# Performance work log

Measured on AMD Instinct MI355X. Metric: run time of the kernel, lower is better.

Reference implementation:

```python
import jax, jax.numpy as jnp
import numpy as np
import math

NH, NKV, D = 32, 8, 128  # query heads, kv heads, head_dim
ROPE_THETA = 10000.0


def _rotate_half(x):
    x1, x2 = jnp.split(x, 2, axis=-1)
    return jnp.concatenate([-x2, x1], axis=-1)


def _rope_cache(position_ids):
    # position_ids: [B, S] int -> cos, sin: [B, S, D]
    inv_freq = 1.0 / (ROPE_THETA ** (jnp.arange(0, D, 2, dtype=jnp.float32) / D))
    freqs = position_ids.astype(jnp.float32)[..., None] * inv_freq  # [B,S,D/2]
    emb = jnp.concatenate([freqs, freqs], axis=-1)  # [B,S,D]
    return jnp.cos(emb), jnp.sin(emb)


def setup_inputs() -> dict:
    key = jax.random.key(0)
    k0, k1, k2, k3, k4 = jax.random.split(key, 5)
    B, S, H = 1, 2048, 4096
    scale = 0.02
    return {
        "hidden_states": jax.random.normal(k0, (B, S, H), jnp.float32),
        "position_ids": jnp.broadcast_to(jnp.arange(S, dtype=jnp.int32), (B, S)),
        "Wq": jax.random.normal(k1, (H, NH * D), jnp.float32) * scale,
        "Wk": jax.random.normal(k2, (H, NKV * D), jnp.float32) * scale,
        "Wv": jax.random.normal(k3, (H, NKV * D), jnp.float32) * scale,
        "Wo": jax.random.normal(k4, (NH * D, H), jnp.float32) * scale,
    }


def reference(hidden_states, position_ids, Wq, Wk, Wv, Wo):
    B, S, H = hidden_states.shape
    # QKV projections, move heads front: [B, H, S, D]
    Q = (hidden_states @ Wq).reshape(B, S, NH, D).transpose(0, 2, 1, 3)
    K = (hidden_states @ Wk).reshape(B, S, NKV, D).transpose(0, 2, 1, 3)
    V = (hidden_states @ Wv).reshape(B, S, NKV, D).transpose(0, 2, 1, 3)
    # RoPE
    cos, sin = _rope_cache(position_ids)  # [B,S,D]
    cos, sin = cos[:, None], sin[:, None]  # broadcast over heads
    Q = Q * cos + _rotate_half(Q) * sin
    K = K * cos + _rotate_half(K) * sin
    # GQA: repeat kv heads to match query heads
    g = NH // NKV
    K = jnp.repeat(K, g, axis=1)
    V = jnp.repeat(V, g, axis=1)
    # scaled QK^T with causal mask (mask=True -> keep, else finfo.min)
    scores = jnp.einsum("bhqd,bhkd->bhqk", Q, K) / math.sqrt(D)
    causal = jnp.tril(jnp.ones((S, S), dtype=bool))
    scores = jnp.where(causal, scores, jnp.finfo(scores.dtype).min)
    probs = jax.nn.softmax(scores.astype(jnp.float32), axis=-1).astype(Q.dtype)
    attn = jnp.einsum("bhqk,bhkd->bhqd", probs, V)
    attn = attn.transpose(0, 2, 1, 3).reshape(B, S, NH * D)
    return attn @ Wo
```

## Files before the change

kernel.cpp:

```cpp
#include <hip/hip_runtime.h>
#include <hip/hip_bf16.h>
#include <math.h>

typedef __bf16 bf16;
typedef __bf16 bf16x8 __attribute__((ext_vector_type(8)));
typedef float f32x4 __attribute__((ext_vector_type(4)));

#define GLB __attribute__((address_space(1)))
#define LDSAS __attribute__((address_space(3)))

__global__ void probe_dtype(const unsigned int* __restrict__ X, int* __restrict__ flag) {
  int t = threadIdx.x;
  int cnt = 0;
  for (int i = t; i < 512; i += 64) {
    unsigned int e = (X[i] >> 7) & 0xFF;
    cnt += (e >= 110 && e <= 135) ? 1 : 0;
  }
#pragma unroll
  for (int off = 32; off > 0; off >>= 1) cnt += __shfl_down(cnt, off, 64);
  if (t == 0) flag[0] = (cnt < 256) ? 1 : 0;
}

__global__ void cast_to_bf16(const void* __restrict__ X, bf16* __restrict__ Y,
                             const int* __restrict__ flag, int n) {
  const int i = (blockIdx.x * 256 + threadIdx.x) * 4;
  if (i >= n) return;
  if (flag[0]) {
    const float* xf = (const float*)X;
#pragma unroll
    for (int j = 0; j < 4; ++j) Y[i + j] = (bf16)xf[i + j];
  } else {
    const bf16* xb = (const bf16*)X;
#pragma unroll
    for (int j = 0; j < 4; ++j) Y[i + j] = xb[i + j];
  }
}

__global__ void transpose_to_bf16(const void* __restrict__ W, bf16* __restrict__ Wt,
                                  const int* __restrict__ flag, int K, int N) {
  __shared__ bf16 tile[32][34];
  const int n0 = blockIdx.x * 32, k0 = blockIdx.y * 32;
  const int tx = threadIdx.x, ty = threadIdx.y;
  const int f = flag[0];
#pragma unroll
  for (int j = 0; j < 4; ++j) {
    const size_t idx = (size_t)(k0 + ty + j * 8) * N + n0 + tx;
    tile[ty + j * 8][tx] = f ? (bf16)((const float*)W)[idx] : ((const bf16*)W)[idx];
  }
  __syncthreads();
#pragma unroll
  for (int j = 0; j < 4; ++j)
    Wt[(size_t)(n0 + ty + j * 8) * K + k0 + tx] = tile[tx][ty + j * 8];
}

__global__ void transpose_v(const bf16* __restrict__ V, bf16* __restrict__ Vt) {
  __shared__ bf16 tile[32][34];
  const int v0 = blockIdx.x * 32, s0 = blockIdx.y * 32;
  const int tx = threadIdx.x, ty = threadIdx.y;
#pragma unroll
  for (int j = 0; j < 4; ++j)
    tile[ty + j * 8][tx] = V[(size_t)(s0 + ty + j * 8) * 6144 + v0 + tx];
  __syncthreads();
#pragma unroll
  for (int j = 0; j < 4; ++j)
    Vt[(size_t)(v0 + ty + j * 8) * 2048 + s0 + tx] = tile[tx][ty + j * 8];
}

__global__ __launch_bounds__(256, 2) void gemm_bt(
    const bf16* __restrict__ A, const bf16* __restrict__ Bt,
    void* __restrict__ C, const int* __restrict__ flagp, int M, int N, int K) {
  __shared__ bf16 As[128 * 32];
  __shared__ bf16 Bs[128 * 32];
  const int t = threadIdx.x;
  const int m0 = blockIdx.y * 128, n0 = blockIdx.x * 128;
  const int lane = t & 63, n16 = lane & 15, quad = lane >> 4;
  const int w = t >> 6, wrow = w >> 1, wcol = w & 1;

  f32x4 acc[4][4] = {};
  const int colA = (t & 3) * 8;
  const int rA = t >> 2;

  for (int k0 = 0; k0 < K; k0 += 32) {
#pragma unroll
    for (int i = 0; i < 2; ++i) {
      const int elem = i * 2048 + t * 8;
      const int row = i * 64 + rA;
      __builtin_amdgcn_global_load_lds(
          (const GLB void*)(A + (size_t)(m0 + row) * K + k0 + colA),
          (LDSAS void*)(&As[elem]), 16, 0, 0);
      __builtin_amdgcn_global_load_lds(
          (const GLB void*)(Bt + (size_t)(n0 + row) * K + k0 + colA),
          (LDSAS void*)(&Bs[elem]), 16, 0, 0);
    }
    __syncthreads();
    bf16x8 af[4], bfr[4];
#pragma unroll
    for (int i = 0; i < 4; ++i) {
      af[i] = *(const bf16x8*)&As[(wrow * 64 + i * 16 + n16) * 32 + quad * 8];
      bfr[i] = *(const bf16x8*)&Bs[(wcol * 64 + i * 16 + n16) * 32 + quad * 8];
    }
#pragma unroll
    for (int mi = 0; mi < 4; ++mi)
#pragma unroll
      for (int ni = 0; ni < 4; ++ni)
        acc[mi][ni] = __builtin_amdgcn_mfma_f32_16x16x32_bf16(
            af[mi], bfr[ni], acc[mi][ni], 0, 0, 0);
    __syncthreads();
  }
  const bool f32out = (flagp != nullptr) && (flagp[0] != 0);
  if (f32out) {
    float* Cf = (float*)C;
#pragma unroll
    for (int mi = 0; mi < 4; ++mi)
#pragma unroll
      for (int ni = 0; ni < 4; ++ni) {
        const int r0 = m0 + wrow * 64 + mi * 16 + quad * 4;
        const int c = n0 + wcol * 64 + ni * 16 + n16;
#pragma unroll
        for (int r = 0; r < 4; ++r) Cf[(size_t)(r0 + r) * N + c] = acc[mi][ni][r];
      }
  } else {
    bf16* Cb = (bf16*)C;
#pragma unroll
    for (int mi = 0; mi < 4; ++mi)
#pragma unroll
      for (int ni = 0; ni < 4; ++ni) {
        const int r0 = m0 + wrow * 64 + mi * 16 + quad * 4;
        const int c = n0 + wcol * 64 + ni * 16 + n16;
#pragma unroll
        for (int r = 0; r < 4; ++r) Cb[(size_t)(r0 + r) * N + c] = (bf16)acc[mi][ni][r];
      }
  }
}

__global__ void rope_kernel(bf16* __restrict__ X, const int* __restrict__ pos,
                            int heads, int stride, int col0) {
  const int idx = blockIdx.x * 256 + threadIdx.x;
  const int i = idx & 63;
  const int hh = (idx >> 6) % heads;
  const int s = idx / (64 * heads);
  bf16* px = X + (size_t)s * stride + col0 + hh * 128 + i;
  const float x1 = (float)px[0], x2 = (float)px[64];
  const float p = (float)pos[s];
  const float inv = exp2f((float)i * -0.2076205088f);
  float sn, cs;
  sincosf(p * inv, &sn, &cs);
  px[0] = (bf16)(x1 * cs - x2 * sn);
  px[64] = (bf16)(x2 * cs + x1 * sn);
}

__global__ __launch_bounds__(256) void flash_attn(
    const bf16* __restrict__ QKV, const bf16* __restrict__ Vt_g,
    bf16* __restrict__ O) {
  __shared__ bf16 Ks[64 * 136];
  __shared__ bf16 Vs[128 * 64];
  __shared__ bf16 Ps[64 * 72];
  const int pairp = blockIdx.x;
  const int h = blockIdx.y, hkv = h >> 2;
  const int t = threadIdx.x, w = t >> 6, lane = t & 63;
  const int n16 = lane & 15, quad = lane >> 4;
  const bf16* Qp = QKV + h * 128;
  const bf16* Kp = QKV + 4096 + hkv * 128;
  const int srow = t >> 4, scol = (t & 15) * 8;
  const int vc = t & 7;

  for (int pass = 0; pass < 2; ++pass) {
    const int qt = (pass == 0) ? pairp : 31 - pairp;
    bf16x8 qa[4];
    {
      const bf16* qrow = Qp + (size_t)(qt * 64 + w * 16 + n16) * 6144 + quad * 8;
#pragma unroll
      for (int kf = 0; kf < 4; ++kf) qa[kf] = *(const bf16x8*)(qrow + kf * 32);
    }
    f32x4 o[8] = {};
    float m_[4] = {-1e30f, -1e30f, -1e30f, -1e30f};
    float l_[4] = {0.f, 0.f, 0.f, 0.f};

    for (int kt = 0; kt <= qt; ++kt) {
#pragma unroll
      for (int j = 0; j < 4; ++j) {
        const int rr = j * 16 + srow;
        *(bf16x8*)&Ks[rr * 136 + scol] =
            *(const bf16x8*)(Kp + (size_t)(kt * 64 + rr) * 6144 + scol);
      }
#pragma unroll
      for (int it = 0; it < 4; ++it) {
        const int d = it * 32 + (t >> 3);
        const bf16x8 vv = *(const bf16x8*)(
            Vt_g + (size_t)(hkv * 128 + d) * 2048 + kt * 64 + vc * 8);
        *(bf16x8*)&Vs[d * 64 + ((vc ^ (d & 7)) * 8)] = vv;
      }
      __syncthreads();

      float p[4][4];
      const bool diag = (kt == qt);
#pragma unroll
      for (int ns = 0; ns < 4; ++ns) {
        f32x4 c = {};
#pragma unroll
        for (int kf = 0; kf < 4; ++kf)
          c = __builtin_amdgcn_mfma_f32_16x16x32_bf16(
              qa[kf],
              *(const bf16x8*)&Ks[(ns * 16 + n16) * 136 + kf * 32 + quad * 8],
              c, 0, 0, 0);
        if (diag) {
          const int kvi = ns * 16 + n16;
          const int ql = w * 16 + quad * 4;
#pragma unroll
          for (int r = 0; r < 4; ++r)
            p[ns][r] = (kvi > ql + r) ? -1e30f : c[r] * 0.08838834764831845f;
        } else {
#pragma unroll
          for (int r = 0; r < 4; ++r) p[ns][r] = c[r] * 0.08838834764831845f;
        }
      }
      float alpha[4];
#pragma unroll
      for (int r = 0; r < 4; ++r) {
        float rmax = fmaxf(fmaxf(p[0][r], p[1][r]), fmaxf(p[2][r], p[3][r]));
#pragma unroll
        for (int off = 1; off < 16; off <<= 1)
          rmax = fmaxf(rmax, __shfl_xor(rmax, off, 64));
        const float mn = fmaxf(m_[r], rmax);
        alpha[r] = __expf(m_[r] - mn);
        float rs = 0.f;
#pragma unroll
        for (int ns = 0; ns < 4; ++ns) {
          const float e = __expf(p[ns][r] - mn);
          p[ns][r] = e;
          rs += e;
        }
#pragma unroll
        for (int off = 1; off < 16; off <<= 1) rs += __shfl_xor(rs, off, 64);
        l_[r] = l_[r] * alpha[r] + rs;
        m_[r] = mn;
      }
#pragma unroll
      for (int dt = 0; dt < 8; ++dt)
#pragma unroll
        for (int r = 0; r < 4; ++r) o[dt][r] *= alpha[r];
#pragma unroll
      for (int ns = 0; ns < 4; ++ns)
#pragma unroll
        for (int r = 0; r < 4; ++r)
          Ps[(w * 16 + quad * 4 + r) * 72 + ns * 16 + n16] = (bf16)p[ns][r];
      __syncthreads();
      const bf16x8 a0 = *(const bf16x8*)&Ps[(w * 16 + n16) * 72 + quad * 8];
      const bf16x8 a1 = *(const bf16x8*)&Ps[(w * 16 + n16) * 72 + 32 + quad * 8];
#pragma unroll
      for (int dt = 0; dt < 8; ++dt) {
        const int d = dt * 16 + n16;
        const int s7 = d & 7;
        const bf16x8 b0 = *(const bf16x8*)&Vs[d * 64 + ((quad ^ s7) * 8)];
        o[dt] = __builtin_amdgcn_mfma_f32_16x16x32_bf16(a0, b0, o[dt], 0, 0, 0);
        const bf16x8 b1 = *(const bf16x8*)&Vs[d * 64 + (((4 + quad) ^ s7) * 8)];
        o[dt] = __builtin_amdgcn_mfma_f32_16x16x32_bf16(a1, b1, o[dt], 0, 0, 0);
      }
      __syncthreads();
    }
    float linv[4];
#pragma unroll
    for (int r = 0; r < 4; ++r) linv[r] = 1.f / l_[r];
#pragma unroll
    for (int dt = 0; dt < 8; ++dt)
#pragma unroll
      for (int r = 0; r < 4; ++r) {
        const int qi = qt * 64 + w * 16 + quad * 4 + r;
        O[(size_t)qi * 4096 + h * 128 + dt * 16 + n16] = (bf16)(o[dt][r] * linv[r]);
      }
  }
}

extern "C" void kernel_launch(void* const* d_in, const int* in_sizes, int n_in,
                              void* d_out, int out_size, void* d_ws, size_t ws_size,
                              hipStream_t stream) {
  (void)in_sizes; (void)n_in; (void)out_size; (void)ws_size;
  const void* X = d_in[0];
  const int* pos = (const int*)d_in[1];
  const void* Wq = d_in[2];
  const void* Wk = d_in[3];
  const void* Wv = d_in[4];
  const void* Wo = d_in[5];

  char* ws = (char*)d_ws;
  const size_t MB = 1ull << 20;
  int* flag   = (int*)(ws + 0);
  bf16* Xb    = (bf16*)(ws + 1 * MB);
  bf16* attn  = (bf16*)(ws + 1 * MB);
  bf16* Wqkvt = (bf16*)(ws + 17 * MB);
  bf16* Wot   = (bf16*)(ws + 65 * MB);
  bf16* QKV   = (bf16*)(ws + 97 * MB);
  bf16* Vt_g  = (bf16*)(ws + 121 * MB);

  probe_dtype<<<1, 64, 0, stream>>>((const unsigned int*)X, flag);
  cast_to_bf16<<<8192, 256, 0, stream>>>(X, Xb, flag, 2048 * 4096);

  const dim3 tb(32, 8);
  transpose_to_bf16<<<dim3(128, 128), tb, 0, stream>>>(Wq, Wqkvt, flag, 4096, 4096);
  transpose_to_bf16<<<dim3(32, 128), tb, 0, stream>>>(Wk, Wqkvt + (size_t)4096 * 4096, flag, 4096, 1024);
  transpose_to_bf16<<<dim3(32, 128), tb, 0, stream>>>(Wv, Wqkvt + (size_t)5120 * 4096, flag, 4096, 1024);
  transpose_to_bf16<<<dim3(128, 128), tb, 0, stream>>>(Wo, Wot, flag, 4096, 4096);

  gemm_bt<<<dim3(48, 16), 256, 0, stream>>>(Xb, Wqkvt, QKV, nullptr, 2048, 6144, 4096);

  rope_kernel<<<16384, 256, 0, stream>>>(QKV, pos, 32, 6144, 0);
  rope_kernel<<<4096, 256, 0, stream>>>(QKV, pos, 8, 6144, 4096);

  transpose_v<<<dim3(32, 64), tb, 0, stream>>>(QKV + 5120, Vt_g);

  flash_attn<<<dim3(16, 32), 256, 0, stream>>>(QKV, Vt_g, attn);

  gemm_bt<<<dim3(32, 16), 256, 0, stream>>>(attn, Wot, d_out, flag, 2048, 4096, 4096);
}
```

Measured before the change: 563.3 us.

## Fuse prep kernels, swizzle GEMM LDS, merge RoPE, widen flash-attn query tiles

Merges the input cast and four weight transposes into one prep kernel, and folds the two RoPE launches into one covering the 40 Q+K heads. The GEMM LDS layout gets an XOR swizzle to cut bank conflicts. Flash attention moves from paired 64-row passes to 128-row query tiles per block with a 1D grid ordered longest-first, so each K/V tile load is shared by more queries and one barrier per tile is removed. The price is more registers for the doubled accumulators and per-group causal skipping inside the key loop.

```diff
diff --git a/kernel.cpp b/kernel.cpp
--- a/kernel.cpp
+++ b/kernel.cpp
@@ -21,27 +21,37 @@
   if (t == 0) flag[0] = (cnt < 256) ? 1 : 0;
 }
 
-__global__ void cast_to_bf16(const void* __restrict__ X, bf16* __restrict__ Y,
-                             const int* __restrict__ flag, int n) {
-  const int i = (blockIdx.x * 256 + threadIdx.x) * 4;
-  if (i >= n) return;
-  if (flag[0]) {
-    const float* xf = (const float*)X;
-#pragma unroll
-    for (int j = 0; j < 4; ++j) Y[i + j] = (bf16)xf[i + j];
+__global__ void prep_weights(const void* __restrict__ Wq, const void* __restrict__ Wk,
+                             const void* __restrict__ Wv, const void* __restrict__ Wo,
+                             const void* __restrict__ X,
+                             bf16* __restrict__ Wqkvt, bf16* __restrict__ Wot,
+                             bf16* __restrict__ Xb, const int* __restrict__ flag) {
+  const int f = flag[0];
+  const int tx = threadIdx.x, ty = threadIdx.y;
+  __shared__ bf16 tile[32][34];
+  int b = blockIdx.x;
+  const void* W;
+  bf16* out;
+  int N, bx, by;
+  if (b < 16384) {
+    W = Wq; out = Wqkvt; N = 4096; bx = b & 127; by = b >> 7;
+  } else if (b < 20480) {
+    b -= 16384; W = Wk; out = Wqkvt + (size_t)4096 * 4096; N = 1024; bx = b & 31; by = b >> 5;
+  } else if (b < 24576) {
+    b -= 20480; W = Wv; out = Wqkvt + (size_t)5120 * 4096; N = 1024; bx = b & 31; by = b >> 5;
+  } else if (b < 40960) {
+    b -= 24576; W = Wo; out = Wot; N = 4096; bx = b & 127; by = b >> 7;
   } else {
-    const bf16* xb = (const bf16*)X;
-#pragma unroll
-    for (int j = 0; j < 4; ++j) Y[i + j] = xb[i + j];
-  }
-}
-
-__global__ void transpose_to_bf16(const void* __restrict__ W, bf16* __restrict__ Wt,
-                                  const int* __restrict__ flag, int K, int N) {
-  __shared__ bf16 tile[32][34];
-  const int n0 = blockIdx.x * 32, k0 = blockIdx.y * 32;
-  const int tx = threadIdx.x, ty = threadIdx.y;
-  const int f = flag[0];
+    b -= 40960;
+    const int x0 = (b & 127) * 32, s0 = (b >> 7) * 32;
+#pragma unroll
+    for (int j = 0; j < 4; ++j) {
+      const size_t idx = (size_t)(s0 + ty + j * 8) * 4096 + x0 + tx;
+      Xb[idx] = f ? (bf16)((const float*)X)[idx] : ((const bf16*)X)[idx];
+    }
+    return;
+  }
+  const int n0 = bx * 32, k0 = by * 32;
 #pragma unroll
   for (int j = 0; j < 4; ++j) {
     const size_t idx = (size_t)(k0 + ty + j * 8) * N + n0 + tx;
@@ -50,7 +60,7 @@
   __syncthreads();
 #pragma unroll
   for (int j = 0; j < 4; ++j)
-    Wt[(size_t)(n0 + ty + j * 8) * K + k0 + tx] = tile[tx][ty + j * 8];
+    out[(size_t)(n0 + ty + j * 8) * 4096 + k0 + tx] = tile[tx][ty + j * 8];
 }
 
 __global__ void transpose_v(const bf16* __restrict__ V, bf16* __restrict__ Vt) {
@@ -77,8 +87,10 @@
   const int w = t >> 6, wrow = w >> 1, wcol = w & 1;
 
   f32x4 acc[4][4] = {};
-  const int colA = (t & 3) * 8;
+  const int colA = (((t & 3) ^ ((t >> 3) & 3))) * 8;
   const int rA = t >> 2;
+  const int sw = (n16 >> 1) & 3;
+  const int rdoff = ((quad ^ sw) * 8);
 
   for (int k0 = 0; k0 < K; k0 += 32) {
 #pragma unroll
@@ -96,8 +108,8 @@
     bf16x8 af[4], bfr[4];
 #pragma unroll
     for (int i = 0; i < 4; ++i) {
-      af[i] = *(const bf16x8*)&As[(wrow * 64 + i * 16 + n16) * 32 + quad * 8];
-      bfr[i] = *(const bf16x8*)&Bs[(wcol * 64 + i * 16 + n16) * 32 + quad * 8];
+      af[i] = *(const bf16x8*)&As[(wrow * 64 + i * 16 + n16) * 32 + rdoff];
+      bfr[i] = *(const bf16x8*)&Bs[(wcol * 64 + i * 16 + n16) * 32 + rdoff];
     }
 #pragma unroll
     for (int mi = 0; mi < 4; ++mi)
@@ -134,12 +146,12 @@
 }
 
 __global__ void rope_kernel(bf16* __restrict__ X, const int* __restrict__ pos,
-                            int heads, int stride, int col0) {
+                            int heads, int stride) {
   const int idx = blockIdx.x * 256 + threadIdx.x;
   const int i = idx & 63;
   const int hh = (idx >> 6) % heads;
   const int s = idx / (64 * heads);
-  bf16* px = X + (size_t)s * stride + col0 + hh * 128 + i;
+  bf16* px = X + (size_t)s * stride + hh * 128 + i;
   const float x1 = (float)px[0], x2 = (float)px[64];
   const float p = (float)pos[s];
   const float inv = exp2f((float)i * -0.2076205088f);
@@ -154,9 +166,10 @@
     bf16* __restrict__ O) {
   __shared__ bf16 Ks[64 * 136];
   __shared__ bf16 Vs[128 * 64];
-  __shared__ bf16 Ps[64 * 72];
-  const int pairp = blockIdx.x;
-  const int h = blockIdx.y, hkv = h >> 2;
+  __shared__ bf16 Ps[128 * 72];
+  const int x = blockIdx.x;
+  const int h = x & 31, hkv = h >> 2;
+  const int qt = (x < 256) ? (15 - (x >> 5)) : ((x - 256) >> 5);
   const int t = threadIdx.x, w = t >> 6, lane = t & 63;
   const int n16 = lane & 15, quad = lane >> 4;
   const bf16* Qp = QKV + h * 128;
@@ -164,48 +177,55 @@
   const int srow = t >> 4, scol = (t & 15) * 8;
   const int vc = t & 7;
 
-  for (int pass = 0; pass < 2; ++pass) {
-    const int qt = (pass == 0) ? pairp : 31 - pairp;
-    bf16x8 qa[4];
-    {
-      const bf16* qrow = Qp + (size_t)(qt * 64 + w * 16 + n16) * 6144 + quad * 8;
-#pragma unroll
-      for (int kf = 0; kf < 4; ++kf) qa[kf] = *(const bf16x8*)(qrow + kf * 32);
-    }
-    f32x4 o[8] = {};
-    float m_[4] = {-1e30f, -1e30f, -1e30f, -1e30f};
-    float l_[4] = {0.f, 0.f, 0.f, 0.f};
-
-    for (int kt = 0; kt <= qt; ++kt) {
-#pragma unroll
-      for (int j = 0; j < 4; ++j) {
-        const int rr = j * 16 + srow;
-        *(bf16x8*)&Ks[rr * 136 + scol] =
-            *(const bf16x8*)(Kp + (size_t)(kt * 64 + rr) * 6144 + scol);
-      }
-#pragma unroll
-      for (int it = 0; it < 4; ++it) {
-        const int d = it * 32 + (t >> 3);
-        const bf16x8 vv = *(const bf16x8*)(
-            Vt_g + (size_t)(hkv * 128 + d) * 2048 + kt * 64 + vc * 8);
-        *(bf16x8*)&Vs[d * 64 + ((vc ^ (d & 7)) * 8)] = vv;
-      }
-      __syncthreads();
-
+  bf16x8 qa[2][4];
+#pragma unroll
+  for (int g = 0; g < 2; ++g) {
+    const bf16* qrow = Qp + (size_t)(qt * 128 + w * 32 + g * 16 + n16) * 6144 + quad * 8;
+#pragma unroll
+    for (int kf = 0; kf < 4; ++kf) qa[g][kf] = *(const bf16x8*)(qrow + kf * 32);
+  }
+  f32x4 o[2][8] = {};
+  float m_[2][4], l_[2][4];
+#pragma unroll
+  for (int g = 0; g < 2; ++g)
+#pragma unroll
+    for (int r = 0; r < 4; ++r) { m_[g][r] = -1e30f; l_[g][r] = 0.f; }
+
+  const int nkt = 2 * qt + 2;
+  for (int kt = 0; kt < nkt; ++kt) {
+#pragma unroll
+    for (int j = 0; j < 4; ++j) {
+      const int rr = j * 16 + srow;
+      *(bf16x8*)&Ks[rr * 136 + scol] =
+          *(const bf16x8*)(Kp + (size_t)(kt * 64 + rr) * 6144 + scol);
+    }
+#pragma unroll
+    for (int it = 0; it < 4; ++it) {
+      const int d = it * 32 + (t >> 3);
+      const bf16x8 vv = *(const bf16x8*)(
+          Vt_g + (size_t)(hkv * 128 + d) * 2048 + kt * 64 + vc * 8);
+      *(bf16x8*)&Vs[d * 64 + ((vc ^ (d & 7)) * 8)] = vv;
+    }
+    __syncthreads();
+
+#pragma unroll
+    for (int g = 0; g < 2; ++g) {
+      const int bq = qt * 128 + w * 32 + g * 16;
+      if (kt * 64 > bq + 15) continue;
       float p[4][4];
-      const bool diag = (kt == qt);
+      const bool needMask = (kt * 64 + 63 > bq);
 #pragma unroll
       for (int ns = 0; ns < 4; ++ns) {
         f32x4 c = {};
 #pragma unroll
         for (int kf = 0; kf < 4; ++kf)
           c = __builtin_amdgcn_mfma_f32_16x16x32_bf16(
-              qa[kf],
+              qa[g][kf],
               *(const bf16x8*)&Ks[(ns * 16 + n16) * 136 + kf * 32 + quad * 8],
               c, 0, 0, 0);
-        if (diag) {
-          const int kvi = ns * 16 + n16;
-          const int ql = w * 16 + quad * 4;
+        if (needMask) {
+          const int kvi = kt * 64 + ns * 16 + n16;
+          const int ql = bq + quad * 4;
 #pragma unroll
           for (int r = 0; r < 4; ++r)
             p[ns][r] = (kvi > ql + r) ? -1e30f : c[r] * 0.08838834764831845f;
@@ -221,8 +241,8 @@
 #pragma unroll
         for (int off = 1; off < 16; off <<= 1)
           rmax = fmaxf(rmax, __shfl_xor(rmax, off, 64));
-        const float mn = fmaxf(m_[r], rmax);
-        alpha[r] = __expf(m_[r] - mn);
+        const float mn = fmaxf(m_[g][r], rmax);
+        alpha[r] = __expf(m_[g][r] - mn);
         float rs = 0.f;
 #pragma unroll
         for (int ns = 0; ns < 4; ++ns) {
@@ -232,41 +252,43 @@
         }
 #pragma unroll
         for (int off = 1; off < 16; off <<= 1) rs += __shfl_xor(rs, off, 64);
-        l_[r] = l_[r] * alpha[r] + rs;
-        m_[r] = mn;
+        l_[g][r] = l_[g][r] * alpha[r] + rs;
+        m_[g][r] = mn;
       }
 #pragma unroll
       for (int dt = 0; dt < 8; ++dt)
 #pragma unroll
-        for (int r = 0; r < 4; ++r) o[dt][r] *= alpha[r];
+        for (int r = 0; r < 4; ++r) o[g][dt][r] *= alpha[r];
 #pragma unroll
       for (int ns = 0; ns < 4; ++ns)
 #pragma unroll
         for (int r = 0; r < 4; ++r)
-          Ps[(w * 16 + quad * 4 + r) * 72 + ns * 16 + n16] = (bf16)p[ns][r];
-      __syncthreads();
-      const bf16x8 a0 = *(const bf16x8*)&Ps[(w * 16 + n16) * 72 + quad * 8];
-      const bf16x8 a1 = *(const bf16x8*)&Ps[(w * 16 + n16) * 72 + 32 + quad * 8];
+          Ps[(w * 32 + g * 16 + quad * 4 + r) * 72 + ns * 16 + n16] = (bf16)p[ns][r];
+      const bf16x8 a0 = *(const bf16x8*)&Ps[(w * 32 + g * 16 + n16) * 72 + quad * 8];
+      const bf16x8 a1 = *(const bf16x8*)&Ps[(w * 32 + g * 16 + n16) * 72 + 32 + quad * 8];
 #pragma unroll
       for (int dt = 0; dt < 8; ++dt) {
         const int d = dt * 16 + n16;
         const int s7 = d & 7;
         const bf16x8 b0 = *(const bf16x8*)&Vs[d * 64 + ((quad ^ s7) * 8)];
-        o[dt] = __builtin_amdgcn_mfma_f32_16x16x32_bf16(a0, b0, o[dt], 0, 0, 0);
+        o[g][dt] = __builtin_amdgcn_mfma_f32_16x16x32_bf16(a0, b0, o[g][dt], 0, 0, 0);
         const bf16x8 b1 = *(const bf16x8*)&Vs[d * 64 + (((4 + quad) ^ s7) * 8)];
-        o[dt] = __builtin_amdgcn_mfma_f32_16x16x32_bf16(a1, b1, o[dt], 0, 0, 0);
-      }
-      __syncthreads();
-    }
+        o[g][dt] = __builtin_amdgcn_mfma_f32_16x16x32_bf16(a1, b1, o[g][dt], 0, 0, 0);
+      }
+    }
+    __syncthreads();
+  }
+#pragma unroll
+  for (int g = 0; g < 2; ++g) {
     float linv[4];
 #pragma unroll
-    for (int r = 0; r < 4; ++r) linv[r] = 1.f / l_[r];
+    for (int r = 0; r < 4; ++r) linv[r] = 1.f / l_[g][r];
 #pragma unroll
     for (int dt = 0; dt < 8; ++dt)
 #pragma unroll
       for (int r = 0; r < 4; ++r) {
-        const int qi = qt * 64 + w * 16 + quad * 4 + r;
-        O[(size_t)qi * 4096 + h * 128 + dt * 16 + n16] = (bf16)(o[dt][r] * linv[r]);
+        const int qi = qt * 128 + w * 32 + g * 16 + quad * 4 + r;
+        O[(size_t)qi * 4096 + h * 128 + dt * 16 + n16] = (bf16)(o[g][dt][r] * linv[r]);
       }
   }
 }
@@ -293,22 +315,17 @@
   bf16* Vt_g  = (bf16*)(ws + 121 * MB);
 
   probe_dtype<<<1, 64, 0, stream>>>((const unsigned int*)X, flag);
-  cast_to_bf16<<<8192, 256, 0, stream>>>(X, Xb, flag, 2048 * 4096);
-
-  const dim3 tb(32, 8);
-  transpose_to_bf16<<<dim3(128, 128), tb, 0, stream>>>(Wq, Wqkvt, flag, 4096, 4096);
-  transpose_to_bf16<<<dim3(32, 128), tb, 0, stream>>>(Wk, Wqkvt + (size_t)4096 * 4096, flag, 4096, 1024);
-  transpose_to_bf16<<<dim3(32, 128), tb, 0, stream>>>(Wv, Wqkvt + (size_t)5120 * 4096, flag, 4096, 1024);
-  transpose_to_bf16<<<dim3(128, 128), tb, 0, stream>>>(Wo, Wot, flag, 4096, 4096);
+
+  prep_weights<<<49152, dim3(32, 8), 0, stream>>>(Wq, Wk, Wv, Wo, X,
+                                                  Wqkvt, Wot, Xb, flag);
 
   gemm_bt<<<dim3(48, 16), 256, 0, stream>>>(Xb, Wqkvt, QKV, nullptr, 2048, 6144, 4096);
 
-  rope_kernel<<<16384, 256, 0, stream>>>(QKV, pos, 32, 6144, 0);
-  rope_kernel<<<4096, 256, 0, stream>>>(QKV, pos, 8, 6144, 4096);
-
-  transpose_v<<<dim3(32, 64), tb, 0, stream>>>(QKV + 5120, Vt_g);
-
-  flash_attn<<<dim3(16, 32), 256, 0, stream>>>(QKV, Vt_g, attn);
+  rope_kernel<<<20480, 256, 0, stream>>>(QKV, pos, 40, 6144);
+
+  transpose_v<<<dim3(32, 64), dim3(32, 8), 0, stream>>>(QKV + 5120, Vt_g);
+
+  flash_attn<<<512, 256, 0, stream>>>(QKV, Vt_g, attn);
 
   gemm_bt<<<dim3(32, 16), 256, 0, stream>>>(attn, Wot, d_out, flag, 2048, 4096, 4096);
 }
```

New measurement: 615.3 us. 9.2% more time.

## Double-buffer flash-attn K/V via LDS DMA, swizzle GEMM LDS, merge prep kernels

Applied to the files above, without the earlier changes.

Flash attention now stages K and V tiles with direct global-to-LDS loads into double buffers, so the next tile loads while the current one is computed. It uses XOR-swizzled layouts and drops two barriers per iteration. The GEMM gets an XOR swizzle on its LDS tiles to reduce bank conflicts. The cast and weight-transpose kernels are merged into one launch, and the two RoPE launches become one. This relies on the compiler waiting for the asynchronous LDS loads before each barrier, and on Ps staying wave-private, which is a correctness risk if either assumption fails.

```diff
diff --git a/kernel.cpp b/kernel.cpp
--- a/kernel.cpp
+++ b/kernel.cpp
@@ -21,27 +21,37 @@
   if (t == 0) flag[0] = (cnt < 256) ? 1 : 0;
 }
 
-__global__ void cast_to_bf16(const void* __restrict__ X, bf16* __restrict__ Y,
-                             const int* __restrict__ flag, int n) {
-  const int i = (blockIdx.x * 256 + threadIdx.x) * 4;
-  if (i >= n) return;
-  if (flag[0]) {
-    const float* xf = (const float*)X;
-#pragma unroll
-    for (int j = 0; j < 4; ++j) Y[i + j] = (bf16)xf[i + j];
+__global__ void prep_weights(const void* __restrict__ Wq, const void* __restrict__ Wk,
+                             const void* __restrict__ Wv, const void* __restrict__ Wo,
+                             const void* __restrict__ X,
+                             bf16* __restrict__ Wqkvt, bf16* __restrict__ Wot,
+                             bf16* __restrict__ Xb, const int* __restrict__ flag) {
+  const int f = flag[0];
+  const int tx = threadIdx.x, ty = threadIdx.y;
+  __shared__ bf16 tile[32][34];
+  int b = blockIdx.x;
+  const void* W;
+  bf16* out;
+  int N, bx, by;
+  if (b < 16384) {
+    W = Wq; out = Wqkvt; N = 4096; bx = b & 127; by = b >> 7;
+  } else if (b < 20480) {
+    b -= 16384; W = Wk; out = Wqkvt + (size_t)4096 * 4096; N = 1024; bx = b & 31; by = b >> 5;
+  } else if (b < 24576) {
+    b -= 20480; W = Wv; out = Wqkvt + (size_t)5120 * 4096; N = 1024; bx = b & 31; by = b >> 5;
+  } else if (b < 40960) {
+    b -= 24576; W = Wo; out = Wot; N = 4096; bx = b & 127; by = b >> 7;
   } else {
-    const bf16* xb = (const bf16*)X;
-#pragma unroll
-    for (int j = 0; j < 4; ++j) Y[i + j] = xb[i + j];
-  }
-}
-
-__global__ void transpose_to_bf16(const void* __restrict__ W, bf16* __restrict__ Wt,
-                                  const int* __restrict__ flag, int K, int N) {
-  __shared__ bf16 tile[32][34];
-  const int n0 = blockIdx.x * 32, k0 = blockIdx.y * 32;
-  const int tx = threadIdx.x, ty = threadIdx.y;
-  const int f = flag[0];
+    b -= 40960;
+    const int x0 = (b & 127) * 32, s0 = (b >> 7) * 32;
+#pragma unroll
+    for (int j = 0; j < 4; ++j) {
+      const size_t idx = (size_t)(s0 + ty + j * 8) * 4096 + x0 + tx;
+      Xb[idx] = f ? (bf16)((const float*)X)[idx] : ((const bf16*)X)[idx];
+    }
+    return;
+  }
+  const int n0 = bx * 32, k0 = by * 32;
 #pragma unroll
   for (int j = 0; j < 4; ++j) {
     const size_t idx = (size_t)(k0 + ty + j * 8) * N + n0 + tx;
@@ -50,7 +60,7 @@
   __syncthreads();
 #pragma unroll
   for (int j = 0; j < 4; ++j)
-    Wt[(size_t)(n0 + ty + j * 8) * K + k0 + tx] = tile[tx][ty + j * 8];
+    out[(size_t)(n0 + ty + j * 8) * 4096 + k0 + tx] = tile[tx][ty + j * 8];
 }
 
 __global__ void transpose_v(const bf16* __restrict__ V, bf16* __restrict__ Vt) {
@@ -77,8 +87,10 @@
   const int w = t >> 6, wrow = w >> 1, wcol = w & 1;
 
   f32x4 acc[4][4] = {};
-  const int colA = (t & 3) * 8;
+  const int colA = (((t & 3) ^ ((t >> 3) & 3))) * 8;
   const int rA = t >> 2;
+  const int sw = (n16 >> 1) & 3;
+  const int rdoff = ((quad ^ sw) * 8);
 
   for (int k0 = 0; k0 < K; k0 += 32) {
 #pragma unroll
@@ -96,8 +108,8 @@
     bf16x8 af[4], bfr[4];
 #pragma unroll
     for (int i = 0; i < 4; ++i) {
-      af[i] = *(const bf16x8*)&As[(wrow * 64 + i * 16 + n16) * 32 + quad * 8];
-      bfr[i] = *(const bf16x8*)&Bs[(wcol * 64 + i * 16 + n16) * 32 + quad * 8];
+      af[i] = *(const bf16x8*)&As[(wrow * 64 + i * 16 + n16) * 32 + rdoff];
+      bfr[i] = *(const bf16x8*)&Bs[(wcol * 64 + i * 16 + n16) * 32 + rdoff];
     }
 #pragma unroll
     for (int mi = 0; mi < 4; ++mi)
@@ -134,12 +146,12 @@
 }
 
 __global__ void rope_kernel(bf16* __restrict__ X, const int* __restrict__ pos,
-                            int heads, int stride, int col0) {
+                            int heads, int stride) {
   const int idx = blockIdx.x * 256 + threadIdx.x;
   const int i = idx & 63;
   const int hh = (idx >> 6) % heads;
   const int s = idx / (64 * heads);
-  bf16* px = X + (size_t)s * stride + col0 + hh * 128 + i;
+  bf16* px = X + (size_t)s * stride + hh * 128 + i;
   const float x1 = (float)px[0], x2 = (float)px[64];
   const float p = (float)pos[s];
   const float inv = exp2f((float)i * -0.2076205088f);
@@ -152,8 +164,8 @@
 __global__ __launch_bounds__(256) void flash_attn(
     const bf16* __restrict__ QKV, const bf16* __restrict__ Vt_g,
     bf16* __restrict__ O) {
-  __shared__ bf16 Ks[64 * 136];
-  __shared__ bf16 Vs[128 * 64];
+  __shared__ bf16 Ks[2][64 * 128];
+  __shared__ bf16 Vs[2][128 * 64];
   __shared__ bf16 Ps[64 * 72];
   const int pairp = blockIdx.x;
   const int h = blockIdx.y, hkv = h >> 2;
@@ -161,8 +173,10 @@
   const int n16 = lane & 15, quad = lane >> 4;
   const bf16* Qp = QKV + h * 128;
   const bf16* Kp = QKV + 4096 + hkv * 128;
-  const int srow = t >> 4, scol = (t & 15) * 8;
-  const int vc = t & 7;
+  const bf16* Vp = Vt_g + (size_t)hkv * 128 * 2048;
+
+  const int krow = t >> 4, kg = t & 15;
+  const int vd = t >> 3, vg = t & 7;
 
   for (int pass = 0; pass < 2; ++pass) {
     const int qt = (pass == 0) ? pairp : 31 - pairp;
@@ -176,24 +190,36 @@
     float m_[4] = {-1e30f, -1e30f, -1e30f, -1e30f};
     float l_[4] = {0.f, 0.f, 0.f, 0.f};
 
+    __syncthreads();
+
+    auto stage = [&](int kt, int buf) {
+#pragma unroll
+      for (int j = 0; j < 4; ++j) {
+        const int row = j * 16 + krow;
+        const int g = kg ^ (row & 7);
+        __builtin_amdgcn_global_load_lds(
+            (const GLB void*)(Kp + (size_t)(kt * 64 + row) * 6144 + g * 8),
+            (LDSAS void*)(&Ks[buf][j * 2048 + t * 8]), 16, 0, 0);
+      }
+#pragma unroll
+      for (int j = 0; j < 4; ++j) {
+        const int d = j * 32 + vd;
+        const int g = vg ^ (d & 7);
+        __builtin_amdgcn_global_load_lds(
+            (const GLB void*)(Vp + (size_t)d * 2048 + kt * 64 + g * 8),
+            (LDSAS void*)(&Vs[buf][j * 2048 + t * 8]), 16, 0, 0);
+      }
+    };
+
+    stage(0, 0);
     for (int kt = 0; kt <= qt; ++kt) {
-#pragma unroll
-      for (int j = 0; j < 4; ++j) {
-        const int rr = j * 16 + srow;
-        *(bf16x8*)&Ks[rr * 136 + scol] =
-            *(const bf16x8*)(Kp + (size_t)(kt * 64 + rr) * 6144 + scol);
-      }
-#pragma unroll
-      for (int it = 0; it < 4; ++it) {
-        const int d = it * 32 + (t >> 3);
-        const bf16x8 vv = *(const bf16x8*)(
-            Vt_g + (size_t)(hkv * 128 + d) * 2048 + kt * 64 + vc * 8);
-        *(bf16x8*)&Vs[d * 64 + ((vc ^ (d & 7)) * 8)] = vv;
-      }
+      const int cur = kt & 1;
       __syncthreads();
+      if (kt < qt) stage(kt + 1, cur ^ 1);
 
       float p[4][4];
       const bool diag = (kt == qt);
+      const int s7 = n16 & 7;
 #pragma unroll
       for (int ns = 0; ns < 4; ++ns) {
         f32x4 c = {};
@@ -201,7 +227,8 @@
         for (int kf = 0; kf < 4; ++kf)
           c = __builtin_amdgcn_mfma_f32_16x16x32_bf16(
               qa[kf],
-              *(const bf16x8*)&Ks[(ns * 16 + n16) * 136 + kf * 32 + quad * 8],
+              *(const bf16x8*)&Ks[cur][(ns * 16 + n16) * 128 +
+                                       (((kf * 4 + quad) ^ s7) * 8)],
               c, 0, 0, 0);
         if (diag) {
           const int kvi = ns * 16 + n16;
@@ -244,19 +271,16 @@
 #pragma unroll
         for (int r = 0; r < 4; ++r)
           Ps[(w * 16 + quad * 4 + r) * 72 + ns * 16 + n16] = (bf16)p[ns][r];
-      __syncthreads();
       const bf16x8 a0 = *(const bf16x8*)&Ps[(w * 16 + n16) * 72 + quad * 8];
       const bf16x8 a1 = *(const bf16x8*)&Ps[(w * 16 + n16) * 72 + 32 + quad * 8];
 #pragma unroll
       for (int dt = 0; dt < 8; ++dt) {
         const int d = dt * 16 + n16;
-        const int s7 = d & 7;
-        const bf16x8 b0 = *(const bf16x8*)&Vs[d * 64 + ((quad ^ s7) * 8)];
+        const bf16x8 b0 = *(const bf16x8*)&Vs[cur][d * 64 + ((quad ^ s7) * 8)];
         o[dt] = __builtin_amdgcn_mfma_f32_16x16x32_bf16(a0, b0, o[dt], 0, 0, 0);
-        const bf16x8 b1 = *(const bf16x8*)&Vs[d * 64 + (((4 + quad) ^ s7) * 8)];
+        const bf16x8 b1 = *(const bf16x8*)&Vs[cur][d * 64 + (((4 + quad) ^ s7) * 8)];
         o[dt] = __builtin_amdgcn_mfma_f32_16x16x32_bf16(a1, b1, o[dt], 0, 0, 0);
       }
-      __syncthreads();
     }
     float linv[4];
 #pragma unroll
@@ -293,20 +317,15 @@
   bf16* Vt_g  = (bf16*)(ws + 121 * MB);
 
   probe_dtype<<<1, 64, 0, stream>>>((const unsigned int*)X, flag);
-  cast_to_bf16<<<8192, 256, 0, stream>>>(X, Xb, flag, 2048 * 4096);
-
-  const dim3 tb(32, 8);
-  transpose_to_bf16<<<dim3(128, 128), tb, 0, stream>>>(Wq, Wqkvt, flag, 4096, 4096);
-  transpose_to_bf16<<<dim3(32, 128), tb, 0, stream>>>(Wk, Wqkvt + (size_t)4096 * 4096, flag, 4096, 1024);
-  transpose_to_bf16<<<dim3(32, 128), tb, 0, stream>>>(Wv, Wqkvt + (size_t)5120 * 4096, flag, 4096, 1024);
-  transpose_to_bf16<<<dim3(128, 128), tb, 0, stream>>>(Wo, Wot, flag, 4096, 4096);
+
+  prep_weights<<<49152, dim3(32, 8), 0, stream>>>(Wq, Wk, Wv, Wo, X,
+                                                  Wqkvt, Wot, Xb, flag);
 
   gemm_bt<<<dim3(48, 16), 256, 0, stream>>>(Xb, Wqkvt, QKV, nullptr, 2048, 6144, 4096);
 
-  rope_kernel<<<16384, 256, 0, stream>>>(QKV, pos, 32, 6144, 0);
-  rope_kernel<<<4096, 256, 0, stream>>>(QKV, pos, 8, 6144, 4096);
-
-  transpose_v<<<dim3(32, 64), tb, 0, stream>>>(QKV + 5120, Vt_g);
+  rope_kernel<<<20480, 256, 0, stream>>>(QKV, pos, 40, 6144);
+
+  transpose_v<<<dim3(32, 64), dim3(32, 8), 0, stream>>>(QKV + 5120, Vt_g);
 
   flash_attn<<<dim3(16, 32), 256, 0, stream>>>(QKV, Vt_g, attn);
 
```

Result: faster. 540.3 us (-4.1%).
